# Kernel tuning notes

Hardware: AMD Instinct MI355X
Metric: run time of the kernel (lower is better)

The kernel has to match this reference:

```python
import jax, jax.numpy as jnp
import numpy as np

N, NUM_MEM, HIDDEN = 131072, 1024, 256
TEMPERATURE = 0.5
EPS = 1e-12  # matches F.normalize default eps


def setup_inputs() -> dict:
    key = jax.random.key(0)
    k1, k2 = jax.random.split(key)
    x = jax.random.normal(k1, (N, HIDDEN), dtype=jnp.float32)
    # xavier_uniform-style init for the memory bank
    limit = float(np.sqrt(6.0 / (NUM_MEM + HIDDEN)))
    memories = jax.random.uniform(k2, (NUM_MEM, HIDDEN), dtype=jnp.float32,
                                  minval=-limit, maxval=limit)
    return {"x": x, "memories": memories}


def reference(x, memories):
    # cosine similarity: normalize both sides, then QK^T
    x_norm = x / jnp.maximum(jnp.linalg.norm(x, axis=-1, keepdims=True), EPS)
    mem_norm = memories / jnp.maximum(
        jnp.linalg.norm(memories, axis=-1, keepdims=True), EPS)
    logits = jnp.einsum('nd,md->nm', x_norm, mem_norm) / TEMPERATURE
    weight = jax.nn.softmax(logits, axis=-1)        # [N, num_memories]
    read = jnp.einsum('nm,md->nd', weight, memories)  # weighted memory read
    return read
```

## Files before the change

### kernel.cpp

```cpp
#include <hip/hip_runtime.h>
#include <hip/hip_bf16.h>
#include <stdint.h>

#define HIDDEN 256
#define NMEM   1024
#define LOG2E  1.44269504088896340736f

typedef __attribute__((ext_vector_type(8))) short bf16x8;
typedef __attribute__((ext_vector_type(4))) float f32x4;
typedef unsigned short ushort_t;
typedef unsigned int   uint_t;

__device__ __forceinline__ ushort_t f2bf(float f) {
  uint_t u = __builtin_bit_cast(uint_t, f);
  u += 0x7FFFu + ((u >> 16) & 1u);
  return (ushort_t)(u >> 16);
}

__device__ __forceinline__ void gload_lds16(const void* g, void* l) {
  __builtin_amdgcn_global_load_lds(
      (const __attribute__((address_space(1))) uint_t*)g,
      (__attribute__((address_space(3))) uint_t*)l, 16, 0, 0);
}

__global__ void prep_kernel(const float* __restrict__ mem,
                            ushort_t* __restrict__ wsm,
                            ushort_t* __restrict__ wsv) {
  const int m = blockIdx.x;
  const int k = threadIdx.x;
  float v = mem[m * HIDDEN + k];
  float ss = v * v;
  #pragma unroll
  for (int off = 1; off < 64; off <<= 1) ss += __shfl_xor(ss, off);
  __shared__ float red[4];
  if ((k & 63) == 0) red[k >> 6] = ss;
  __syncthreads();
  const float tot = red[0] + red[1] + red[2] + red[3];
  const float inv = 1.0f / fmaxf(sqrtf(tot), 1e-12f);
  const ushort_t hn = f2bf(v * inv);
  const ushort_t hv = f2bf(v);
  const int t = m >> 5, ml = m & 31;
  const int c = k >> 3;
  wsm[t * 8192 + ((ml * 32 + (c ^ (ml & 7))) << 3) + (k & 7)] = hn;
  const int c2 = ml >> 3;
  wsv[t * 8192 + ((k * 4 + (c2 ^ ((k >> 1) & 3))) << 3) + (ml & 7)] = hv;
}

__global__ __launch_bounds__(256, 2) void mem_kernel(
    const float* __restrict__ x, const ushort_t* __restrict__ wsm,
    const ushort_t* __restrict__ wsv, float* __restrict__ out) {
  __shared__ __align__(16) char lds[70656];
  const int tid  = threadIdx.x;
  const int lane = tid & 63;
  const int wave = tid >> 6;
  const int g    = lane >> 4;
  const int lr   = lane & 15;
  const int row0 = blockIdx.x * 64 + wave * 16;

  float xf[64];
  const float* xrow = x + (size_t)(row0 + lr) * HIDDEN + g * 8;
  #pragma unroll
  for (int kt = 0; kt < 8; ++kt) {
    float4 a = *(const float4*)(xrow + kt * 32);
    float4 b = *(const float4*)(xrow + kt * 32 + 4);
    xf[kt*8+0]=a.x; xf[kt*8+1]=a.y; xf[kt*8+2]=a.z; xf[kt*8+3]=a.w;
    xf[kt*8+4]=b.x; xf[kt*8+5]=b.y; xf[kt*8+6]=b.z; xf[kt*8+7]=b.w;
  }
  float ss = 0.f;
  #pragma unroll
  for (int i = 0; i < 64; ++i) ss += xf[i] * xf[i];
  ss += __shfl_xor(ss, 16);
  ss += __shfl_xor(ss, 32);
  const float scale = (2.0f * LOG2E) / fmaxf(sqrtf(ss), 1e-12f);
  bf16x8 ax[8];
  #pragma unroll
  for (int kt = 0; kt < 8; ++kt) {
    #pragma unroll
    for (int j = 0; j < 8; ++j) ax[kt][j] = (short)f2bf(xf[kt*8+j] * scale);
  }

  const char* gm = (const char*)wsm;
  const char* gv = (const char*)wsv;
  auto stage = [&](int t, int buf) {
    const int base = buf * 32768;
    #pragma unroll
    for (int i = 0; i < 4; ++i) {
      const int off = wave * 4096 + i * 1024;
      gload_lds16(gm + t * 16384 + off + lane * 16, lds + base + off);
      gload_lds16(gv + t * 16384 + off + lane * 16, lds + base + 16384 + off);
    }
  };

  f32x4 o[16];
  const f32x4 z4 = {0.f, 0.f, 0.f, 0.f};
  #pragma unroll
  for (int i = 0; i < 16; ++i) o[i] = z4;
  float den[4] = {0.f, 0.f, 0.f, 0.f};

  const int xr = lr & 7;
  const int hk = (xr >> 2) & 1;
  const int gx = (g ^ (xr & 3)) << 4;
  const int g2 = (g ^ ((lr >> 1) & 3)) << 4;
  const uint_t pbase = 65536u + (uint_t)wave * 1280u;

  stage(0, 0);
  __syncthreads();

  for (int t = 0; t < 32; ++t) {
    const int buf = t & 1;
    if (t < 31) stage(t + 1, buf ^ 1);
    const int mbase = buf * 32768;
    const int vbase = mbase + 16384;

    float pf[8];
    #pragma unroll
    for (int half = 0; half < 2; ++half) {
      const int ml = half * 16 + lr;
      const char* mrb = lds + mbase + ml * 512 + gx;
      f32x4 s = z4;
      #pragma unroll
      for (int kt = 0; kt < 8; ++kt) {
        bf16x8 bfrag = *(const bf16x8*)(mrb + (((kt ^ hk) << 6)));
        s = __builtin_amdgcn_mfma_f32_16x16x32_bf16(ax[kt], bfrag, s, 0, 0, 0);
      }
      #pragma unroll
      for (int r = 0; r < 4; ++r) {
        const float p = exp2f(s[r]);
        den[r] += p;
        pf[half * 4 + r] = p;
      }
    }

    ushort_t* pw = (ushort_t*)(lds + pbase);
    #pragma unroll
    for (int half = 0; half < 2; ++half) {
      #pragma unroll
      for (int r = 0; r < 4; ++r)
        pw[(4 * g + r) * 40 + half * 16 + lr] = f2bf(pf[half * 4 + r]);
    }
    asm volatile("s_waitcnt lgkmcnt(0)" ::: "memory");
    __builtin_amdgcn_sched_barrier(0);
    const bf16x8 pa = *(const bf16x8*)(lds + pbase + lr * 80 + g * 16);

    const char* vrb = lds + vbase + lr * 64 + g2;
    #pragma unroll
    for (int d0 = 0; d0 < 16; ++d0) {
      bf16x8 vfrag = *(const bf16x8*)(vrb + d0 * 1024);
      o[d0] = __builtin_amdgcn_mfma_f32_16x16x32_bf16(pa, vfrag, o[d0], 0, 0, 0);
    }
    __syncthreads();
  }

  #pragma unroll
  for (int r = 0; r < 4; ++r) {
    den[r] += __shfl_xor(den[r], 1);
    den[r] += __shfl_xor(den[r], 2);
    den[r] += __shfl_xor(den[r], 4);
    den[r] += __shfl_xor(den[r], 8);
  }

  float* op = out + (size_t)(row0 + 4 * g) * HIDDEN + lr;
  #pragma unroll
  for (int r = 0; r < 4; ++r) {
    const float rd = 1.0f / den[r];
    #pragma unroll
    for (int d0 = 0; d0 < 16; ++d0)
      op[r * HIDDEN + d0 * 16] = o[d0][r] * rd;
  }
}

extern "C" void kernel_launch(void* const* d_in, const int* in_sizes, int n_in,
                              void* d_out, int out_size, void* d_ws, size_t ws_size,
                              hipStream_t stream) {
  const float* x   = (const float*)d_in[0];
  const float* mem = (const float*)d_in[1];
  float* out = (float*)d_out;
  const int N = in_sizes[0] / HIDDEN;

  ushort_t* wsm = (ushort_t*)d_ws;
  ushort_t* wsv = wsm + NMEM * HIDDEN;

  prep_kernel<<<NMEM, HIDDEN, 0, stream>>>(mem, wsm, wsv);
  mem_kernel<<<N / 64, 256, 0, stream>>>(x, wsm, wsv, out);
}
```

Before: 383.6 us.

## Switch to 32x32x16 MFMA with 256-row blocks and in-register P transpose

Moves the fused attention-style kernel from 16x16x32 to 32x32x16 bf16 MFMA. Each block now has 8 waves covering 256 rows and stages 64-memory tiles of both the normalized and raw memory bank into 128KB of double-buffered LDS, and the prep kernel's swizzled layout changes to match. The LDS round trip for the softmax probabilities is replaced by v_permlane32_swap, so they become MFMA A-operands directly, and the extra LDS barrier goes away. The aim is to cut LDS traffic and instruction overhead per FLOP. In exchange it needs a large LDS footprint, which limits occupancy, and raises register pressure.

```diff
diff --git a/kernel.cpp b/kernel.cpp
--- a/kernel.cpp
+++ b/kernel.cpp
@@ -6,8 +6,8 @@
 #define NMEM   1024
 #define LOG2E  1.44269504088896340736f
 
-typedef __attribute__((ext_vector_type(8))) short bf16x8;
-typedef __attribute__((ext_vector_type(4))) float f32x4;
+typedef __attribute__((ext_vector_type(8)))  short bf16x8;
+typedef __attribute__((ext_vector_type(16))) float f32x16;
 typedef unsigned short ushort_t;
 typedef unsigned int   uint_t;
 
@@ -39,133 +39,137 @@
   const float inv = 1.0f / fmaxf(sqrtf(tot), 1e-12f);
   const ushort_t hn = f2bf(v * inv);
   const ushort_t hv = f2bf(v);
-  const int t = m >> 5, ml = m & 31;
-  const int c = k >> 3;
-  wsm[t * 8192 + ((ml * 32 + (c ^ (ml & 7))) << 3) + (k & 7)] = hn;
-  const int c2 = ml >> 3;
-  wsv[t * 8192 + ((k * 4 + (c2 ^ ((k >> 1) & 3))) << 3) + (ml & 7)] = hv;
+  const int t = m >> 6, mr = m & 63;
+  wsm[t * 16384 + mr * 256 + (((k >> 3) ^ (mr & 7)) << 3) + (k & 7)] = hn;
+  wsv[t * 16384 + k * 64 + (((mr >> 3) ^ (k & 7)) << 3) + (mr & 7)] = hv;
 }
 
-__global__ __launch_bounds__(256, 2) void mem_kernel(
+__global__ __launch_bounds__(512, 2) void mem_kernel(
     const float* __restrict__ x, const ushort_t* __restrict__ wsm,
     const ushort_t* __restrict__ wsv, float* __restrict__ out) {
-  __shared__ __align__(16) char lds[70656];
+  __shared__ __align__(16) char lds[131072];
   const int tid  = threadIdx.x;
   const int lane = tid & 63;
   const int wave = tid >> 6;
-  const int g    = lane >> 4;
-  const int lr   = lane & 15;
-  const int row0 = blockIdx.x * 64 + wave * 16;
+  const int col  = lane & 31;
+  const int hi   = lane >> 5;
+  const int row0 = blockIdx.x * 256 + wave * 32;
+  const char* gm = (const char*)wsm;
+  const char* gv = (const char*)wsv;
 
-  float xf[64];
-  const float* xrow = x + (size_t)(row0 + lr) * HIDDEN + g * 8;
   #pragma unroll
-  for (int kt = 0; kt < 8; ++kt) {
-    float4 a = *(const float4*)(xrow + kt * 32);
-    float4 b = *(const float4*)(xrow + kt * 32 + 4);
-    xf[kt*8+0]=a.x; xf[kt*8+1]=a.y; xf[kt*8+2]=a.z; xf[kt*8+3]=a.w;
-    xf[kt*8+4]=b.x; xf[kt*8+5]=b.y; xf[kt*8+6]=b.z; xf[kt*8+7]=b.w;
+  for (int r = 0; r < 4; ++r) {
+    const int o = r * 8192 + wave * 1024;
+    gload_lds16(gm + o + lane * 16, lds + o);
+    gload_lds16(gv + o + lane * 16, lds + 32768 + o);
+  }
+
+  float xf[16][8];
+  const float* xr = x + (size_t)(row0 + col) * HIDDEN + hi * 8;
+  #pragma unroll
+  for (int ks = 0; ks < 16; ++ks) {
+    float4 a = *(const float4*)(xr + ks * 16);
+    float4 b = *(const float4*)(xr + ks * 16 + 4);
+    xf[ks][0]=a.x; xf[ks][1]=a.y; xf[ks][2]=a.z; xf[ks][3]=a.w;
+    xf[ks][4]=b.x; xf[ks][5]=b.y; xf[ks][6]=b.z; xf[ks][7]=b.w;
   }
   float ss = 0.f;
   #pragma unroll
-  for (int i = 0; i < 64; ++i) ss += xf[i] * xf[i];
-  ss += __shfl_xor(ss, 16);
+  for (int ks = 0; ks < 16; ++ks)
+    #pragma unroll
+    for (int j = 0; j < 8; ++j) ss += xf[ks][j] * xf[ks][j];
   ss += __shfl_xor(ss, 32);
   const float scale = (2.0f * LOG2E) / fmaxf(sqrtf(ss), 1e-12f);
-  bf16x8 ax[8];
+  bf16x8 xb[16];
   #pragma unroll
-  for (int kt = 0; kt < 8; ++kt) {
+  for (int ks = 0; ks < 16; ++ks)
     #pragma unroll
-    for (int j = 0; j < 8; ++j) ax[kt][j] = (short)f2bf(xf[kt*8+j] * scale);
-  }
+    for (int j = 0; j < 8; ++j) xb[ks][j] = (short)f2bf(xf[ks][j] * scale);
 
-  const char* gm = (const char*)wsm;
-  const char* gv = (const char*)wsv;
-  auto stage = [&](int t, int buf) {
-    const int base = buf * 32768;
-    #pragma unroll
-    for (int i = 0; i < 4; ++i) {
-      const int off = wave * 4096 + i * 1024;
-      gload_lds16(gm + t * 16384 + off + lane * 16, lds + base + off);
-      gload_lds16(gv + t * 16384 + off + lane * 16, lds + base + 16384 + off);
-    }
-  };
+  const f32x16 zz = {0.f,0.f,0.f,0.f, 0.f,0.f,0.f,0.f,
+                     0.f,0.f,0.f,0.f, 0.f,0.f,0.f,0.f};
+  f32x16 o8[8];
+  #pragma unroll
+  for (int i = 0; i < 8; ++i) o8[i] = zz;
+  float den = 0.f;
 
-  f32x4 o[16];
-  const f32x4 z4 = {0.f, 0.f, 0.f, 0.f};
-  #pragma unroll
-  for (int i = 0; i < 16; ++i) o[i] = z4;
-  float den[4] = {0.f, 0.f, 0.f, 0.f};
-
-  const int xr = lr & 7;
-  const int hk = (xr >> 2) & 1;
-  const int gx = (g ^ (xr & 3)) << 4;
-  const int g2 = (g ^ ((lr >> 1) & 3)) << 4;
-  const uint_t pbase = 65536u + (uint_t)wave * 1280u;
-
-  stage(0, 0);
   __syncthreads();
 
-  for (int t = 0; t < 32; ++t) {
-    const int buf = t & 1;
-    if (t < 31) stage(t + 1, buf ^ 1);
-    const int mbase = buf * 32768;
-    const int vbase = mbase + 16384;
-
-    float pf[8];
-    #pragma unroll
-    for (int half = 0; half < 2; ++half) {
-      const int ml = half * 16 + lr;
-      const char* mrb = lds + mbase + ml * 512 + gx;
-      f32x4 s = z4;
-      #pragma unroll
-      for (int kt = 0; kt < 8; ++kt) {
-        bf16x8 bfrag = *(const bf16x8*)(mrb + (((kt ^ hk) << 6)));
-        s = __builtin_amdgcn_mfma_f32_16x16x32_bf16(ax[kt], bfrag, s, 0, 0, 0);
-      }
+  for (int t = 0; t < 16; ++t) {
+    const int mb = (t & 1) << 16;
+    const int vbb = mb + 32768;
+    if (t < 15) {
+      const int nb = ((t & 1) ^ 1) << 16;
+      const int go = (t + 1) * 32768;
       #pragma unroll
       for (int r = 0; r < 4; ++r) {
-        const float p = exp2f(s[r]);
-        den[r] += p;
-        pf[half * 4 + r] = p;
+        const int o = r * 8192 + wave * 1024;
+        gload_lds16(gm + go + o + lane * 16, lds + nb + o);
+        gload_lds16(gv + go + o + lane * 16, lds + nb + 32768 + o);
       }
     }
 
-    ushort_t* pw = (ushort_t*)(lds + pbase);
     #pragma unroll
     for (int half = 0; half < 2; ++half) {
+      const char* ab = lds + mb + (half * 32 + col) * 512;
+      const int sk = col & 7;
+      f32x16 s0 = zz, s1 = zz;
       #pragma unroll
-      for (int r = 0; r < 4; ++r)
-        pw[(4 * g + r) * 40 + half * 16 + lr] = f2bf(pf[half * 4 + r]);
-    }
-    asm volatile("s_waitcnt lgkmcnt(0)" ::: "memory");
-    __builtin_amdgcn_sched_barrier(0);
-    const bf16x8 pa = *(const bf16x8*)(lds + pbase + lr * 80 + g * 16);
-
-    const char* vrb = lds + vbase + lr * 64 + g2;
-    #pragma unroll
-    for (int d0 = 0; d0 < 16; ++d0) {
-      bf16x8 vfrag = *(const bf16x8*)(vrb + d0 * 1024);
-      o[d0] = __builtin_amdgcn_mfma_f32_16x16x32_bf16(pa, vfrag, o[d0], 0, 0, 0);
+      for (int ks = 0; ks < 8; ++ks) {
+        bf16x8 a0 = *(const bf16x8*)(ab + (((4*ks + hi) ^ sk) << 4));
+        bf16x8 a1 = *(const bf16x8*)(ab + (((4*ks + 2 + hi) ^ sk) << 4));
+        s0 = __builtin_amdgcn_mfma_f32_32x32x16_bf16(a0, xb[2*ks],   s0, 0,0,0);
+        s1 = __builtin_amdgcn_mfma_f32_32x32x16_bf16(a1, xb[2*ks+1], s1, 0,0,0);
+      }
+      float p[16];
+      #pragma unroll
+      for (int r = 0; r < 16; ++r) {
+        const float pv = exp2f(s0[r] + s1[r]);
+        den += pv;
+        p[r] = pv;
+      }
+      bf16x8 pa[2];
+      #pragma unroll
+      for (int ks = 0; ks < 2; ++ks) {
+        const int b0 = ks * 8;
+        uint_t w0 = (uint_t)f2bf(p[b0+0]) | ((uint_t)f2bf(p[b0+1]) << 16);
+        uint_t w1 = (uint_t)f2bf(p[b0+2]) | ((uint_t)f2bf(p[b0+3]) << 16);
+        uint_t w2 = (uint_t)f2bf(p[b0+4]) | ((uint_t)f2bf(p[b0+5]) << 16);
+        uint_t w3 = (uint_t)f2bf(p[b0+6]) | ((uint_t)f2bf(p[b0+7]) << 16);
+        asm("v_permlane32_swap_b32 %0, %1" : "+v"(w0), "+v"(w2));
+        asm("v_permlane32_swap_b32 %0, %1" : "+v"(w1), "+v"(w3));
+        uint4 u = {w0, w1, w2, w3};
+        pa[ks] = __builtin_bit_cast(bf16x8, u);
+      }
+      #pragma unroll
+      for (int ks = 0; ks < 2; ++ks) {
+        const int c = half * 4 + ks * 2 + hi;
+        #pragma unroll
+        for (int d0 = 0; d0 < 8; ++d0) {
+          const char* vrow = lds + vbb + (d0 * 32 + col) * 128;
+          bf16x8 vf = *(const bf16x8*)(vrow + ((c ^ sk) << 4));
+          o8[d0] = __builtin_amdgcn_mfma_f32_32x32x16_bf16(pa[ks], vf, o8[d0], 0,0,0);
+        }
+      }
     }
     __syncthreads();
   }
 
+  den += __shfl_xor(den, 32);
+  const float rden = 1.0f / den;
+  float rdv[16];
   #pragma unroll
-  for (int r = 0; r < 4; ++r) {
-    den[r] += __shfl_xor(den[r], 1);
-    den[r] += __shfl_xor(den[r], 2);
-    den[r] += __shfl_xor(den[r], 4);
-    den[r] += __shfl_xor(den[r], 8);
-  }
+  for (int r = 0; r < 16; ++r)
+    rdv[r] = __shfl(rden, (r & 3) + 8 * (r >> 2) + 4 * hi);
 
-  float* op = out + (size_t)(row0 + 4 * g) * HIDDEN + lr;
+  float* op = out + (size_t)row0 * HIDDEN;
   #pragma unroll
-  for (int r = 0; r < 4; ++r) {
-    const float rd = 1.0f / den[r];
+  for (int d0 = 0; d0 < 8; ++d0) {
     #pragma unroll
-    for (int d0 = 0; d0 < 16; ++d0)
-      op[r * HIDDEN + d0 * 16] = o[d0][r] * rd;
+    for (int r = 0; r < 16; ++r) {
+      const int rw = (r & 3) + 8 * (r >> 2) + 4 * hi;
+      op[(size_t)rw * HIDDEN + d0 * 32 + col] = o8[d0][r] * rdv[r];
+    }
   }
 }
 
@@ -181,5 +185,5 @@
   ushort_t* wsv = wsm + NMEM * HIDDEN;
 
   prep_kernel<<<NMEM, HIDDEN, 0, stream>>>(mem, wsm, wsv);
-  mem_kernel<<<N / 64, 256, 0, stream>>>(x, wsm, wsv, out);
+  mem_kernel<<<N / 256, 512, 0, stream>>>(x, wsm, wsv, out);
 }
```

New measurement: 436.0 us. 1.14x slower.
